# Kernel optimization log

Hardware: AMD Instinct MI355X
Metric: run time of the kernel (lower is better)

The kernel has to match this reference:

```python
import jax, jax.numpy as jnp
import numpy as np

H = 256       # hidden_dim
DICT = 30     # dict_size
SOS = 1       # symb2int['<sos>']

def gru_cell(x, h, Wih, Whh, bih, bhh):
    # PyTorch GRU cell math
    gi = x @ Wih.T + bih
    gh = h @ Whh.T + bhh
    ir, iz, inn = jnp.split(gi, 3, axis=-1)
    hr, hz, hn = jnp.split(gh, 3, axis=-1)
    r = jax.nn.sigmoid(ir + hr)
    z = jax.nn.sigmoid(iz + hz)
    n = jnp.tanh(inn + r * hn)
    return (1.0 - z) * n + z * h

def run_gru(xs, h0, Wih, Whh, bih, bhh):
    # xs: [T, B, F] -> outputs [T, B, Hc], final hidden [B, Hc]
    def step(h, x):
        h = gru_cell(x, h, Wih, Whh, bih, bhh)
        return h, h
    hT, out = jax.lax.scan(step, h0, xs)
    return out, hT

def setup_inputs() -> dict:
    key = jax.random.key(0)
    ks = jax.random.split(key, 24)
    B, T, L = 128, 512, 64
    se = 1.0 / np.sqrt(H)        # encoder GRU init scale
    sd = 1.0 / np.sqrt(2 * H)    # decoder GRU / linears scale
    def r(k, shape, sc):
        return jax.random.normal(k, shape, jnp.float32) * sc
    return {
        "x": jax.random.normal(ks[0], (B, T, 2), jnp.float32),
        "target_seq": jax.random.randint(ks[1], (B, L), 0, DICT),
        # encoder GRU, forward direction
        "enc_Wih_f": r(ks[2], (3 * H, 2), se), "enc_Whh_f": r(ks[3], (3 * H, H), se),
        "enc_bih_f": r(ks[4], (3 * H,), se),   "enc_bhh_f": r(ks[5], (3 * H,), se),
        # encoder GRU, backward direction
        "enc_Wih_b": r(ks[6], (3 * H, 2), se), "enc_Whh_b": r(ks[7], (3 * H, H), se),
        "enc_bih_b": r(ks[8], (3 * H,), se),   "enc_bhh_b": r(ks[9], (3 * H,), se),
        # decoder embedding + GRU (hidden 2H)
        "emb": r(ks[10], (DICT, H), 1.0),
        "dec_Wih": r(ks[11], (6 * H, H), sd),     "dec_Whh": r(ks[12], (6 * H, 2 * H), sd),
        "dec_bih": r(ks[13], (6 * H,), sd),       "dec_bhh": r(ks[14], (6 * H,), sd),
        # hidden2query, att_combine, fc
        "Wq": r(ks[15], (2 * H, 2 * H), sd), "bq": r(ks[16], (2 * H,), sd),
        "Wc": r(ks[17], (H, 4 * H), sd),     "bc": r(ks[18], (H,), sd),
        "Wf": r(ks[19], (DICT, H), se),      "bf": r(ks[20], (DICT,), se),
    }

def reference(x, target_seq,
              enc_Wih_f, enc_Whh_f, enc_bih_f, enc_bhh_f,
              enc_Wih_b, enc_Whh_b, enc_bih_b, enc_bhh_b,
              emb, dec_Wih, dec_Whh, dec_bih, dec_bhh,
              Wq, bq, Wc, bc, Wf, bf):
    B = x.shape[0]
    xs = jnp.transpose(x, (1, 0, 2))                # [T, B, 2]
    h0 = jnp.zeros((B, H), x.dtype)
    out_f, hf = run_gru(xs, h0, enc_Wih_f, enc_Whh_f, enc_bih_f, enc_bhh_f)
    out_b, hb = run_gru(xs[::-1], h0, enc_Wih_b, enc_Whh_b, enc_bih_b, enc_bhh_b)
    enc_out = jnp.concatenate([out_f, out_b[::-1]], axis=-1)  # [T, B, 2H]
    enc_out = jnp.transpose(enc_out, (1, 0, 2))               # [B, T, 2H]
    hidden = jnp.concatenate([hf, hb], axis=-1)               # [B, 2H]

    # teacher-forced decoder inputs: <sos>, target[0], ..., target[L-2]
    sos = jnp.full((B, 1), SOS, target_seq.dtype)
    toks = jnp.concatenate([sos, target_seq[:, :-1]], axis=1).T  # [L, B]

    def dec_step(h, tok):
        e = emb[tok]                                           # [B, H]
        h = gru_cell(e, h, dec_Wih, dec_Whh, dec_bih, dec_bhh) # [B, 2H]
        q = h @ Wq.T + bq                                      # hidden2query
        w = jax.nn.softmax(jnp.einsum('bh,bth->bt', q, enc_out), axis=-1)
        ctx = jnp.einsum('bt,bth->bh', w, enc_out)             # [B, 2H]
        o = jnp.concatenate([h, ctx], axis=-1) @ Wc.T + bc     # att_combine
        logits = o @ Wf.T + bf                                 # fc
        return h, (logits, w)

    hT, (logits, ws) = jax.lax.scan(dec_step, hidden, toks)
    vec_out = jnp.transpose(logits, (1, 0, 2))   # [B, L, DICT]
    attn = jnp.transpose(ws, (1, 2, 0))          # [B, T, L]
    return vec_out, hT[None], attn
```

## Files before the change

### kernel.cpp

```cpp
#include <hip/hip_runtime.h>
#include <hip/hip_bf16.h>

typedef unsigned int u32;
typedef unsigned short u16;
typedef _Float16 f16;
typedef f16 f16x2 __attribute__((ext_vector_type(2)));

#define BB 128
#define TT 512
#define HE 256
#define G3E 768
#define HD 512
#define G3D 1536
#define LL 64
#define NDICT 30
#define EMBD 256

__device__ __forceinline__ float fexp2(float v){
#if __has_builtin(__builtin_amdgcn_exp2f)
  return __builtin_amdgcn_exp2f(v);
#else
  return exp2f(v);
#endif
}
__device__ __forceinline__ float frcp(float v){
#if __has_builtin(__builtin_amdgcn_rcpf)
  return __builtin_amdgcn_rcpf(v);
#else
  return 1.f/v;
#endif
}
__device__ __forceinline__ float sigm(float v){
  return frcp(1.f + fexp2(-1.4426950408889634f*v));
}
__device__ __forceinline__ float ftanh(float v){
  float e = fexp2(fminf(v, 40.f)*2.8853901631790583f);
  return (e - 1.f)*frcp(e + 1.f);
}
__device__ __forceinline__ u16 f2h(float f){ return __builtin_bit_cast(u16, (f16)f); }
__device__ __forceinline__ float h2f(u16 b){ return (float)__builtin_bit_cast(f16, b); }
__device__ __forceinline__ u32 pkh2(float a, float b){
  u16 lo = __builtin_bit_cast(u16, (f16)a);
  u16 hi = __builtin_bit_cast(u16, (f16)b);
  return (u32)lo | ((u32)hi << 16);
}
__device__ __forceinline__ u32 pkrtz(float a, float b){
  return __builtin_bit_cast(u32, __builtin_amdgcn_cvt_pkrtz(a, b));
}
__device__ __forceinline__ f16x2 bc2(u32 v){ return __builtin_bit_cast(f16x2, v); }

__device__ __forceinline__ void unp8h(uint4 v, float* d){
  f16x2 p;
  p = bc2(v.x); d[0]=(float)p.x; d[1]=(float)p.y;
  p = bc2(v.y); d[2]=(float)p.x; d[3]=(float)p.y;
  p = bc2(v.z); d[4]=(float)p.x; d[5]=(float)p.y;
  p = bc2(v.w); d[6]=(float)p.x; d[7]=(float)p.y;
}
__device__ __forceinline__ ushort4 hpk4(float a, float b, float c, float d){
  ushort4 r; r.x=f2h(a); r.y=f2h(b); r.z=f2h(c); r.w=f2h(d); return r;
}

__device__ __forceinline__ float dot2a(u32 a, u32 b, float c){
  float d;
  asm("v_dot2_f32_f16 %0, %1, %2, %3" : "=v"(d) : "v"(a), "v"(b), "v"(c));
  return d;
}
__device__ __forceinline__ float dot2h(u32 a, u32 b, float acc){
  return dot2a(a, b, acc);
}
__device__ __forceinline__ void dot_u4(uint4 wv, uint4 hv, float& acc){
  acc = dot2a(wv.x, hv.x, acc);
  acc = dot2a(wv.y, hv.y, acc);
  acc = dot2a(wv.z, hv.z, acc);
  acc = dot2a(wv.w, hv.w, acc);
}

#define INNER8P(Q0,Q1)                                                  \
  _Pragma("unroll")                                                     \
  for (int kp = 0; kp < 16; ++kp){                                      \
    uint4 a2 = *(const uint4*)&A2_s[kp*68 + (Q0)*4];                    \
    uint4 b2 = *(const uint4*)&B2_s[kp*68 + (Q1)*4];                    \
    acc[0] =dot2h(a2.x,b2.x,acc[0]);  acc[1] =dot2h(a2.x,b2.y,acc[1]);  \
    acc[2] =dot2h(a2.x,b2.z,acc[2]);  acc[3] =dot2h(a2.x,b2.w,acc[3]);  \
    acc[4] =dot2h(a2.y,b2.x,acc[4]);  acc[5] =dot2h(a2.y,b2.y,acc[5]);  \
    acc[6] =dot2h(a2.y,b2.z,acc[6]);  acc[7] =dot2h(a2.y,b2.w,acc[7]);  \
    acc[8] =dot2h(a2.z,b2.x,acc[8]);  acc[9] =dot2h(a2.z,b2.y,acc[9]);  \
    acc[10]=dot2h(a2.z,b2.z,acc[10]); acc[11]=dot2h(a2.z,b2.w,acc[11]); \
    acc[12]=dot2h(a2.w,b2.x,acc[12]); acc[13]=dot2h(a2.w,b2.y,acc[13]); \
    acc[14]=dot2h(a2.w,b2.z,acc[14]); acc[15]=dot2h(a2.w,b2.w,acc[15]); \
  }

__global__ __launch_bounds__(256) void k_prep_pairT(const float* __restrict__ src,
                                                    u32* __restrict__ dst, int N, int K){
  int idx = blockIdx.x*256 + threadIdx.x;
  int KP = K >> 1;
  if (idx < N*KP){
    int n = idx / KP, kp = idx - n*KP;
    dst[(size_t)kp*N + n] = pkh2(src[(size_t)n*K + 2*kp], src[(size_t)n*K + 2*kp + 1]);
  }
}

__global__ __launch_bounds__(256) void k_prep_wenc(const float* __restrict__ WF,
                                                   const float* __restrict__ WB,
                                                   uint4* __restrict__ dst){
  int idx = blockIdx.x*256 + threadIdx.x;
  int dir = idx / 24576, rem = idx - dir*24576;
  int i = rem / 768, t = rem - i*768;
  int rg = t >> 3, cg = t & 7;
  int r = i >> 2, q = i & 3;
  const float* s = (dir ? WB : WF) + (size_t)(rg*8 + r)*HE + cg*32 + q*8;
  uint4 v; v.x=pkh2(s[0],s[1]); v.y=pkh2(s[2],s[3]); v.z=pkh2(s[4],s[5]); v.w=pkh2(s[6],s[7]);
  dst[idx] = v;
}

__global__ __launch_bounds__(256) void k_prep_wdec(const float* __restrict__ src,
                                                   uint4* __restrict__ dst){
  int idx = blockIdx.x*256 + threadIdx.x;
  int lane = idx & 63;
  int ci = lane & 7, kq = lane >> 3;
  int rest = idx >> 6;
  int u = rest & 7, g = (rest >> 3) % 3, cg = rest / 24;
  int row = g*512 + cg*8 + ci;
  int col = kq*64 + u*8;
  const float* s = src + (size_t)row*HD + col;
  uint4 v; v.x=pkh2(s[0],s[1]); v.y=pkh2(s[2],s[3]); v.z=pkh2(s[4],s[5]); v.w=pkh2(s[6],s[7]);
  dst[idx] = v;
}

__global__ __launch_bounds__(256) void k_gi_tab(const float* __restrict__ emb,
                                                const float* __restrict__ Wih,
                                                const float* __restrict__ bih,
                                                float* __restrict__ gi){
  int v = blockIdx.x, gy = blockIdx.y;
  int g = gy*256 + threadIdx.x;
  __shared__ float e_s[EMBD];
  if (threadIdx.x < EMBD) e_s[threadIdx.x] = emb[(size_t)v*EMBD + threadIdx.x];
  __syncthreads();
  const float4* w4 = (const float4*)(Wih + (size_t)g*EMBD);
  float acc = 0.f;
  #pragma unroll 8
  for (int k = 0; k < EMBD/4; ++k){
    float4 w = w4[k];
    float4 h = *(const float4*)&e_s[k*4];
    acc = fmaf(w.x,h.x,fmaf(w.y,h.y,fmaf(w.z,h.z,fmaf(w.w,h.w,acc))));
  }
  gi[(size_t)v*G3D + g] = acc + bih[g];
}

__global__ __launch_bounds__(256) void k_h0cvt(const float* __restrict__ src,
                                               f16* __restrict__ dst){
  int i = blockIdx.x*256 + threadIdx.x;
  dst[i] = (f16)src[i];
}

__global__ __launch_bounds__(768, 3) void k_enc_p(
    const float* __restrict__ x,
    const uint4* __restrict__ Wp,
    const float* __restrict__ WihF, const float* __restrict__ WihB,
    const float* __restrict__ bihF, const float* __restrict__ bhhF,
    const float* __restrict__ bihB, const float* __restrict__ bhhB,
    u16* __restrict__ enc_out, float* __restrict__ h0out)
{
  const int b   = blockIdx.x >> 1;
  const int dir = blockIdx.x & 1;
  const int j   = threadIdx.x;
  const int cg  = j & 7;
  const float* Wih = dir ? WihB : WihF;
  const float* bih = dir ? bihB : bihF;
  const float* bhh = dir ? bhhB : bhhF;

  __shared__ __align__(16) f16 h_pad[8*40];
  __shared__ float gh[2*HE];
  __shared__ float gin_s[HE], ghn_s[HE];

  uint4 w[32];
  {
    const uint4* wsrc = Wp + (size_t)dir*24576 + j;
    #pragma unroll
    for (int i = 0; i < 32; ++i) w[i] = wsrc[(size_t)i*768];
  }
  const float wv0r = Wih[j*2+0], wv1r = Wih[j*2+1];
  const float bi = bih[j], bh = bhh[j];
  const float badd = bi + bh;
  if (j < HE) h_pad[(j >> 5)*40 + (j & 31)] = (f16)0.f;
  float h_own = 0.f;
  const bool s0 = (cg & 1), s1 = (cg & 2), s2 = (cg & 4);
  __syncthreads();

  for (int t = 0; t < TT; ++t){
    const int tt = dir ? (TT-1-t) : t;
    const float x0 = x[((size_t)b*TT + tt)*2 + 0];
    const float x1 = x[((size_t)b*TT + tt)*2 + 1];

    const uint4* hv = (const uint4*)(h_pad + cg*40);
    uint4 h0 = hv[0], h1 = hv[1], h2 = hv[2], h3 = hv[3];
    float p[8];
    #pragma unroll
    for (int r = 0; r < 8; ++r){
      float a = 0.f;
      dot_u4(w[r*4+0], h0, a);
      dot_u4(w[r*4+1], h1, a);
      dot_u4(w[r*4+2], h2, a);
      dot_u4(w[r*4+3], h3, a);
      p[r] = a;
    }
    float q0 = (s0 ? p[1] : p[0]) + __shfl_xor(s0 ? p[0] : p[1], 1);
    float q1 = (s0 ? p[3] : p[2]) + __shfl_xor(s0 ? p[2] : p[3], 1);
    float q2 = (s0 ? p[5] : p[4]) + __shfl_xor(s0 ? p[4] : p[5], 1);
    float q3 = (s0 ? p[7] : p[6]) + __shfl_xor(s0 ? p[6] : p[7], 1);
    float r0 = (s1 ? q1 : q0) + __shfl_xor(s1 ? q0 : q1, 2);
    float r1 = (s1 ? q3 : q2) + __shfl_xor(s1 ? q2 : q3, 2);
    float tot = (s2 ? r1 : r0) + __shfl_xor(s2 ? r0 : r1, 4);

    const float xp = fmaf(wv0r, x0, wv1r*x1);
    if (j < 2*HE){
      gh[j] = tot + xp + badd;
    } else {
      ghn_s[j-2*HE] = tot + bh;
      gin_s[j-2*HE] = xp + bi;
    }
    __syncthreads();
    if (j < HE){
      float r = sigm(gh[j]);
      float z = sigm(gh[j+HE]);
      float n = ftanh(gin_s[j] + r*ghn_s[j]);
      float hnew = (1.f - z)*n + z*h_own;
      h_own = hnew;
      h_pad[(j >> 5)*40 + (j & 31)] = (f16)hnew;
      enc_out[((size_t)b*TT + tt)*HD + dir*HE + j] = f2h(hnew);
    }
    __syncthreads();
  }
  if (j < HE) h0out[(size_t)b*HD + dir*HE + j] = h_own;
}

__global__ __launch_bounds__(256, 2) void k_dstep(
    const int* __restrict__ tgt, const float* __restrict__ gi_tab,
    const uint4* __restrict__ Wd2, const float* __restrict__ bhh,
    const f16* __restrict__ h_prev, f16* __restrict__ h_next,
    float* __restrict__ Hall, int l)
{
  const int bg = blockIdx.x & 7, cg = blockIdx.x >> 3;
  const int tid = threadIdx.x;
  const int ci = tid & 7, kq = (tid >> 3) & 7, bq = tid >> 6;

  __shared__ __align__(16) f16 h_s[16][8][72];
  __shared__ float p_s[3][16][8][9];
  __shared__ int tok_s[16];

  uint4 w[24];
  {
    const uint4* wp = Wd2 + (size_t)cg*24*64 + (kq*8 + ci);
    #pragma unroll
    for (int i = 0; i < 24; ++i) w[i] = wp[(size_t)i*64];
  }
  {
    const uint4* hsrc = (const uint4*)(h_prev + (size_t)bg*16*HD);
    #pragma unroll
    for (int i = 0; i < 4; ++i){
      int idx = tid + i*256;
      int b = idx >> 6, w4 = idx & 63;
      int kq2 = w4 >> 3, off = w4 & 7;
      *(uint4*)&h_s[b][kq2][off*8] = hsrc[idx];
    }
  }
  if (tid < 16) tok_s[tid] = (l == 0) ? 1 : tgt[(size_t)(bg*16 + tid)*LL + l - 1];
  __syncthreads();

  #pragma unroll
  for (int nb = 0; nb < 4; ++nb){
    const int b = bq*4 + nb;
    const uint4* hv = (const uint4*)&h_s[b][kq][0];
    float x0 = 0.f, x1 = 0.f, x2 = 0.f;
    #pragma unroll
    for (int u = 0; u < 8; ++u){
      uint4 hh = hv[u];
      dot_u4(w[u],      hh, x0);
      dot_u4(w[8 + u],  hh, x1);
      dot_u4(w[16 + u], hh, x2);
    }
    p_s[0][b][ci][kq] = x0;
    p_s[1][b][ci][kq] = x1;
    p_s[2][b][ci][kq] = x2;
  }
  __syncthreads();

  if (tid < 128){
    const int b = tid >> 3, cl = tid & 7;
    const int C = cg*8 + cl;
    float s0 = 0.f, s1 = 0.f, s2 = 0.f;
    #pragma unroll
    for (int k = 0; k < 8; ++k){
      s0 += p_s[0][b][cl][k];
      s1 += p_s[1][b][cl][k];
      s2 += p_s[2][b][cl][k];
    }
    const int tok = tok_s[b];
    const float* gp = gi_tab + (size_t)tok*G3D + C;
    float r = sigm(gp[0]    + s0 + bhh[C]);
    float z = sigm(gp[HD]   + s1 + bhh[HD + C]);
    float n = ftanh(gp[2*HD] + r*(s2 + bhh[2*HD + C]));
    float hp = (float)h_s[b][C >> 6][C & 63];
    float hnew = (1.f - z)*n + z*hp;
    const int gb = bg*16 + b;
    h_next[(size_t)gb*HD + C] = (f16)hnew;
    Hall[((size_t)l*BB + gb)*HD + C] = hnew;
  }
}

__global__ __launch_bounds__(256) void k_query(const float* __restrict__ Hall,
                                               const u32* __restrict__ Wq2,
                                               const float* __restrict__ bq,
                                               u16* __restrict__ Qh){
  const int rt = blockIdx.x, nt = blockIdx.y;
  const int tid = threadIdx.x;
  __shared__ u32 A2_s[16*68];
  __shared__ u32 B2_s[16*68];
  const int rq = tid >> 4, nq = tid & 15;
  const int i = tid >> 2, jj = tid & 3;
  const int i3 = tid >> 4, n4 = tid & 15;
  float acc[16] = {};
  for (int kc = 0; kc < 16; ++kc){
    __syncthreads();
    {
      const float* src = Hall + (size_t)(rt*64 + i)*HD + kc*32 + jj*8;
      float4 v0 = *(const float4*)src, v1 = *(const float4*)(src+4);
      A2_s[(jj*4+0)*68+i] = pkrtz(v0.x, v0.y);
      A2_s[(jj*4+1)*68+i] = pkrtz(v0.z, v0.w);
      A2_s[(jj*4+2)*68+i] = pkrtz(v1.x, v1.y);
      A2_s[(jj*4+3)*68+i] = pkrtz(v1.z, v1.w);
    }
    {
      uint4 v = *(const uint4*)(Wq2 + (size_t)(kc*16 + i3)*HD + nt*64 + n4*4);
      *(uint4*)&B2_s[i3*68 + n4*4] = v;
    }
    __syncthreads();
    INNER8P(rq, nq)
  }
  const int n0 = nt*64 + nq*4;
  float4 bv = *(const float4*)&bq[n0];
  #pragma unroll
  for (int r = 0; r < 4; ++r){
    u16* dst = Qh + (size_t)(rt*64 + rq*4 + r)*HD + n0;
    *(ushort4*)dst = hpk4(acc[r*4+0]+bv.x, acc[r*4+1]+bv.y,
                          acc[r*4+2]+bv.z, acc[r*4+3]+bv.w);
  }
}

__global__ __launch_bounds__(256) void k_scores(const u16* __restrict__ Qh,
                                                const u16* __restrict__ enc,
                                                float* __restrict__ Sbuf){
  const int bI = blockIdx.x, tt = blockIdx.y;
  const int tid = threadIdx.x;
  __shared__ u32 A2_s[16*68];
  __shared__ u32 B2_s[16*68];
  const int lq = tid >> 4, tq = tid & 15;
  const int i = tid >> 2, jj = tid & 3;
  float acc[16] = {};
  for (int kc = 0; kc < 16; ++kc){
    __syncthreads();
    {
      uint4 va = *(const uint4*)(Qh + ((size_t)i*BB + bI)*HD + kc*32 + jj*8);
      A2_s[(jj*4+0)*68+i] = va.x;
      A2_s[(jj*4+1)*68+i] = va.y;
      A2_s[(jj*4+2)*68+i] = va.z;
      A2_s[(jj*4+3)*68+i] = va.w;
    }
    {
      uint4 vb = *(const uint4*)(enc + ((size_t)bI*TT + tt*64 + i)*HD + kc*32 + jj*8);
      B2_s[(jj*4+0)*68+i] = vb.x;
      B2_s[(jj*4+1)*68+i] = vb.y;
      B2_s[(jj*4+2)*68+i] = vb.z;
      B2_s[(jj*4+3)*68+i] = vb.w;
    }
    __syncthreads();
    INNER8P(lq, tq)
  }
  #pragma unroll
  for (int r = 0; r < 4; ++r){
    float4 o = make_float4(acc[r*4+0],acc[r*4+1],acc[r*4+2],acc[r*4+3]);
    *(float4*)&Sbuf[((size_t)bI*LL + lq*4+r)*TT + tt*64 + tq*4] = o;
  }
}

__global__ __launch_bounds__(64) void k_softmax(const float* __restrict__ Sbuf,
                                                u16* __restrict__ Ph){
  const int row = blockIdx.x;
  const int lane = threadIdx.x;
  const float* s = Sbuf + (size_t)row*TT;
  float v[8]; float m = -1e30f;
  #pragma unroll
  for (int i = 0; i < 8; ++i){ v[i] = s[lane + i*64]; m = fmaxf(m, v[i]); }
  #pragma unroll
  for (int o = 32; o; o >>= 1) m = fmaxf(m, __shfl_xor(m, o));
  float Z = 0.f;
  #pragma unroll
  for (int i = 0; i < 8; ++i){ v[i] = fexp2(1.4426950408889634f*(v[i] - m)); Z += v[i]; }
  #pragma unroll
  for (int o = 32; o; o >>= 1) Z += __shfl_xor(Z, o);
  float inv = frcp(Z);
  u16* p = Ph + (size_t)row*TT;
  #pragma unroll
  for (int i = 0; i < 8; ++i) p[lane + i*64] = f2h(v[i]*inv);
}

__global__ __launch_bounds__(256) void k_attn_tr(const u16* __restrict__ Ph,
                                                 float* __restrict__ att){
  const int bI = blockIdx.x, tt = blockIdx.y;
  const int tid = threadIdx.x;
  __shared__ u16 tile[64][72];
  {
    const int i = tid >> 2, jj = tid & 3;
    #pragma unroll
    for (int rep = 0; rep < 2; ++rep){
      int ch = jj + rep*4;
      uint4 v = *(const uint4*)(Ph + ((size_t)bI*LL + i)*TT + tt*64 + ch*8);
      *(uint4*)&tile[i][ch*8] = v;
    }
  }
  __syncthreads();
  const int t = tid >> 2, jl = tid & 3;
  #pragma unroll
  for (int rep = 0; rep < 4; ++rep){
    int l0 = jl*16 + rep*4;
    float4 o;
    o.x = h2f(tile[l0+0][t]); o.y = h2f(tile[l0+1][t]);
    o.z = h2f(tile[l0+2][t]); o.w = h2f(tile[l0+3][t]);
    *(float4*)&att[((size_t)bI*TT + tt*64 + t)*LL + l0] = o;
  }
}

__global__ __launch_bounds__(256) void k_ctx(const u16* __restrict__ Ph,
                                             const u16* __restrict__ enc,
                                             u16* __restrict__ ctxh){
  const int bI = blockIdx.x, nt = blockIdx.y;
  const int tid = threadIdx.x;
  __shared__ u32 A2_s[16*68];
  __shared__ u32 B2_s[16*68];
  const int lq = tid >> 4, nq = tid & 15;
  const int i = tid >> 2, jj = tid & 3;
  const int q = tid >> 4, n4 = tid & 15;
  float acc[16] = {};
  for (int tc = 0; tc < 16; ++tc){
    __syncthreads();
    {
      uint4 va = *(const uint4*)(Ph + ((size_t)bI*LL + i)*TT + tc*32 + jj*8);
      A2_s[(jj*4+0)*68+i] = va.x;
      A2_s[(jj*4+1)*68+i] = va.y;
      A2_s[(jj*4+2)*68+i] = va.z;
      A2_s[(jj*4+3)*68+i] = va.w;
    }
    {
      const int t0 = tc*32 + 2*q;
      const int n0 = nt*64 + n4*4;
      uint2 a = *(const uint2*)(enc + ((size_t)bI*TT + t0)*HD + n0);
      uint2 b = *(const uint2*)(enc + ((size_t)bI*TT + t0 + 1)*HD + n0);
      B2_s[q*68 + n4*4 + 0] = (a.x & 0xffffu) | (b.x << 16);
      B2_s[q*68 + n4*4 + 1] = (a.x >> 16) | (b.x & 0xffff0000u);
      B2_s[q*68 + n4*4 + 2] = (a.y & 0xffffu) | (b.y << 16);
      B2_s[q*68 + n4*4 + 3] = (a.y >> 16) | (b.y & 0xffff0000u);
    }
    __syncthreads();
    INNER8P(lq, nq)
  }
  const int n0 = nt*64 + nq*4;
  #pragma unroll
  for (int r = 0; r < 4; ++r){
    int ll = lq*4 + r;
    u16* dst = ctxh + ((size_t)ll*BB + bI)*HD + n0;
    *(ushort4*)dst = hpk4(acc[r*4+0], acc[r*4+1], acc[r*4+2], acc[r*4+3]);
  }
}

__global__ __launch_bounds__(256) void k_outc(const float* __restrict__ Hall,
                                              const u16* __restrict__ ctxh,
                                              const u32* __restrict__ Wc2,
                                              const float* __restrict__ bc,
                                              float* __restrict__ obuf){
  const int rt = blockIdx.x, nt = blockIdx.y;
  const int tid = threadIdx.x;
  __shared__ u32 A2_s[16*68];
  __shared__ u32 B2_s[16*68];
  const int rq = tid >> 4, nq = tid & 15;
  const int i = tid >> 2, jj = tid & 3;
  const int i3 = tid >> 4, n4 = tid & 15;
  float acc[16] = {};
  for (int kc = 0; kc < 32; ++kc){
    __syncthreads();
    if (kc < 16){
      const float* src = Hall + (size_t)(rt*64 + i)*HD + kc*32 + jj*8;
      float4 v0 = *(const float4*)src, v1 = *(const float4*)(src+4);
      A2_s[(jj*4+0)*68+i] = pkrtz(v0.x, v0.y);
      A2_s[(jj*4+1)*68+i] = pkrtz(v0.z, v0.w);
      A2_s[(jj*4+2)*68+i] = pkrtz(v1.x, v1.y);
      A2_s[(jj*4+3)*68+i] = pkrtz(v1.z, v1.w);
    } else {
      uint4 v = *(const uint4*)(ctxh + (size_t)(rt*64 + i)*HD + (kc-16)*32 + jj*8);
      A2_s[(jj*4+0)*68+i] = v.x;
      A2_s[(jj*4+1)*68+i] = v.y;
      A2_s[(jj*4+2)*68+i] = v.z;
      A2_s[(jj*4+3)*68+i] = v.w;
    }
    {
      uint4 v = *(const uint4*)(Wc2 + (size_t)(kc*16 + i3)*256 + nt*64 + n4*4);
      *(uint4*)&B2_s[i3*68 + n4*4] = v;
    }
    __syncthreads();
    INNER8P(rq, nq)
  }
  const int n0 = nt*64 + nq*4;
  float4 bv = *(const float4*)&bc[n0];
  #pragma unroll
  for (int r = 0; r < 4; ++r){
    float4 o = make_float4(acc[r*4+0]+bv.x, acc[r*4+1]+bv.y,
                           acc[r*4+2]+bv.z, acc[r*4+3]+bv.w);
    *(float4*)&obuf[(size_t)(rt*64 + rq*4 + r)*256 + n0] = o;
  }
}

__global__ __launch_bounds__(256) void k_fc(const float* __restrict__ obuf,
                                            const float* __restrict__ Wf,
                                            const float* __restrict__ bfv,
                                            float* __restrict__ out_vec){
  const int rt = blockIdx.x;
  const int tid = threadIdx.x;
  __shared__ float w_s[30*260];
  for (int rr = 0; rr < 30; ++rr) w_s[rr*260 + tid] = Wf[(size_t)rr*256 + tid];
  __syncthreads();
  const int rl = tid >> 2, dq = tid & 3;
  const int r = rt*64 + rl;
  float acc[8] = {};
  for (int k = 0; k < 256; k += 4){
    float4 o4 = *(const float4*)&obuf[(size_t)r*256 + k];
    #pragma unroll
    for (int jq = 0; jq < 8; ++jq){
      int d = dq*8 + jq;
      if (d < 30){
        float4 w4 = *(const float4*)&w_s[d*260 + k];
        acc[jq] = fmaf(o4.x,w4.x,fmaf(o4.y,w4.y,fmaf(o4.z,w4.z,fmaf(o4.w,w4.w,acc[jq]))));
      }
    }
  }
  const int b = r & 127, l = r >> 7;
  #pragma unroll
  for (int jq = 0; jq < 8; ++jq){
    int d = dq*8 + jq;
    if (d < 30) out_vec[((size_t)b*LL + l)*NDICT + d] = acc[jq] + bfv[d];
  }
}

__global__ __launch_bounds__(256) void k_copy(const float* __restrict__ src,
                                              float* __restrict__ dst, int n){
  int i = blockIdx.x*256 + threadIdx.x;
  if (i < n) dst[i] = src[i];
}

extern "C" void kernel_launch(void* const* d_in, const int* in_sizes, int n_in,
                              void* d_out, int out_size, void* d_ws, size_t ws_size,
                              hipStream_t stream)
{
  const float* x     = (const float*)d_in[0];
  const int*   tgt   = (const int*)  d_in[1];
  const float* eWihF = (const float*)d_in[2];
  const float* eWhhF = (const float*)d_in[3];
  const float* ebihF = (const float*)d_in[4];
  const float* ebhhF = (const float*)d_in[5];
  const float* eWihB = (const float*)d_in[6];
  const float* eWhhB = (const float*)d_in[7];
  const float* ebihB = (const float*)d_in[8];
  const float* ebhhB = (const float*)d_in[9];
  const float* emb   = (const float*)d_in[10];
  const float* dWih  = (const float*)d_in[11];
  const float* dWhh  = (const float*)d_in[12];
  const float* dbih  = (const float*)d_in[13];
  const float* dbhh  = (const float*)d_in[14];
  const float* Wq    = (const float*)d_in[15];
  const float* bq    = (const float*)d_in[16];
  const float* Wc    = (const float*)d_in[17];
  const float* bc    = (const float*)d_in[18];
  const float* Wf    = (const float*)d_in[19];
  const float* bfv   = (const float*)d_in[20];

  char* w = (char*)d_ws;
  uint4* Wpenc = (uint4*)w; w += 786432;
  uint4* Wpdec = (uint4*)w; w += 1572864;
  u32*   Wq2   = (u32*)w;  w += 524288;
  u32*   Wc2   = (u32*)w;  w += 524288;
  float* gi_t  = (float*)w; w += 184320;
  float* h0buf = (float*)w; w += 262144;
  f16*   h16A  = (f16*)w; w += 131072;
  f16*   h16B  = (f16*)w; w += 131072;
  float* Hall  = (float*)w; w += 16777216;
  u16*   Qh    = (u16*)w;
  u16*   Ph    = (u16*)w; w += 8388608;
  float* Sbuf  = (float*)w;
  u16*   ctxh  = (u16*)w; w += 8388608;
  float* obuf  = (float*)w; w += 8388608;
  u16*   ench  = (u16*)w; w += 67108864;

  float* out     = (float*)d_out;
  float* out_vec = out;
  float* out_hT  = out + (size_t)BB*LL*NDICT;
  float* out_att = out_hT + (size_t)BB*HD;

  k_prep_wenc<<<192, 256, 0, stream>>>(eWhhF, eWhhB, Wpenc);
  k_prep_wdec<<<384, 256, 0, stream>>>(dWhh, Wpdec);
  k_prep_pairT<<<512, 256, 0, stream>>>(Wq, Wq2, HD, HD);
  k_prep_pairT<<<512, 256, 0, stream>>>(Wc, Wc2, 256, 1024);
  k_gi_tab<<<dim3(NDICT, 6), 256, 0, stream>>>(emb, dWih, dbih, gi_t);

  k_enc_p<<<BB*2, G3E, 0, stream>>>(x, Wpenc, eWihF, eWihB,
                                    ebihF, ebhhF, ebihB, ebhhB, ench, h0buf);

  k_h0cvt<<<256, 256, 0, stream>>>(h0buf, h16A);
  for (int l = 0; l < LL; ++l){
    const f16* hp = (l & 1) ? h16B : h16A;
    f16*       hn = (l & 1) ? h16A : h16B;
    k_dstep<<<512, 256, 0, stream>>>(tgt, gi_t, Wpdec, dbhh, hp, hn, Hall, l);
  }

  k_query<<<dim3(128,8), 256, 0, stream>>>(Hall, Wq2, bq, Qh);
  k_scores<<<dim3(128,8), 256, 0, stream>>>(Qh, ench, Sbuf);
  k_softmax<<<BB*LL, 64, 0, stream>>>(Sbuf, Ph);
  k_attn_tr<<<dim3(128,8), 256, 0, stream>>>(Ph, out_att);
  k_ctx<<<dim3(128,8), 256, 0, stream>>>(Ph, ench, ctxh);
  k_outc<<<dim3(128,4), 256, 0, stream>>>(Hall, ctxh, Wc2, bc, obuf);
  k_fc<<<BB, 256, 0, stream>>>(obuf, Wf, bfv, out_vec);
  k_copy<<<(BB*HD+255)/256, 256, 0, stream>>>(Hall + (size_t)63*BB*HD, out_hT, BB*HD);
}
```

Measured before the change: 1.244 ms.

## Restructure encoder GRU step to 512 threads with LDS partial-sum reduction

The encoder recurrence kernel moves from 768 to 512 threads per block. Each thread now holds 48 weight vectors and computes 12 gate rows over a 32-column slice. The old shuffle-based reduction is replaced by writing partial dot products to shared memory, after which 256 threads sum them and apply the gate math. This trades more register pressure and extra LDS traffic for fewer waves and no cross-lane shuffles. The weight prep layout and the dot2 helper (now a builtin when available) are updated to match.

```diff
diff --git a/kernel.cpp b/kernel.cpp
--- a/kernel.cpp
+++ b/kernel.cpp
@@ -49,30 +49,24 @@
 }
 __device__ __forceinline__ f16x2 bc2(u32 v){ return __builtin_bit_cast(f16x2, v); }
 
-__device__ __forceinline__ void unp8h(uint4 v, float* d){
-  f16x2 p;
-  p = bc2(v.x); d[0]=(float)p.x; d[1]=(float)p.y;
-  p = bc2(v.y); d[2]=(float)p.x; d[3]=(float)p.y;
-  p = bc2(v.z); d[4]=(float)p.x; d[5]=(float)p.y;
-  p = bc2(v.w); d[6]=(float)p.x; d[7]=(float)p.y;
-}
 __device__ __forceinline__ ushort4 hpk4(float a, float b, float c, float d){
   ushort4 r; r.x=f2h(a); r.y=f2h(b); r.z=f2h(c); r.w=f2h(d); return r;
 }
 
-__device__ __forceinline__ float dot2a(u32 a, u32 b, float c){
+__device__ __forceinline__ float dot2h(u32 a, u32 b, float acc){
+#if __has_builtin(__builtin_amdgcn_fdot2)
+  return __builtin_amdgcn_fdot2(bc2(a), bc2(b), acc, false);
+#else
   float d;
-  asm("v_dot2_f32_f16 %0, %1, %2, %3" : "=v"(d) : "v"(a), "v"(b), "v"(c));
+  asm("v_dot2_f32_f16 %0, %1, %2, %3" : "=v"(d) : "v"(a), "v"(b), "v"(acc));
   return d;
-}
-__device__ __forceinline__ float dot2h(u32 a, u32 b, float acc){
-  return dot2a(a, b, acc);
+#endif
 }
 __device__ __forceinline__ void dot_u4(uint4 wv, uint4 hv, float& acc){
-  acc = dot2a(wv.x, hv.x, acc);
-  acc = dot2a(wv.y, hv.y, acc);
-  acc = dot2a(wv.z, hv.z, acc);
-  acc = dot2a(wv.w, hv.w, acc);
+  acc = dot2h(wv.x, hv.x, acc);
+  acc = dot2h(wv.y, hv.y, acc);
+  acc = dot2h(wv.z, hv.z, acc);
+  acc = dot2h(wv.w, hv.w, acc);
 }
 
 #define INNER8P(Q0,Q1)                                                  \
@@ -105,10 +99,10 @@
                                                    uint4* __restrict__ dst){
   int idx = blockIdx.x*256 + threadIdx.x;
   int dir = idx / 24576, rem = idx - dir*24576;
-  int i = rem / 768, t = rem - i*768;
+  int i = rem >> 9, t = rem & 511;
   int rg = t >> 3, cg = t & 7;
-  int r = i >> 2, q = i & 3;
-  const float* s = (dir ? WB : WF) + (size_t)(rg*8 + r)*HE + cg*32 + q*8;
+  int k = i >> 2, q = i & 3;
+  const float* s = (dir ? WB : WF) + (size_t)(rg*12 + k)*HE + cg*32 + q*8;
   uint4 v; v.x=pkh2(s[0],s[1]); v.y=pkh2(s[2],s[3]); v.z=pkh2(s[4],s[5]); v.w=pkh2(s[6],s[7]);
   dst[idx] = v;
 }
@@ -153,7 +147,7 @@
   dst[i] = (f16)src[i];
 }
 
-__global__ __launch_bounds__(768, 3) void k_enc_p(
+__global__ __launch_bounds__(512, 2) void k_enc_p(
     const float* __restrict__ x,
     const uint4* __restrict__ Wp,
     const float* __restrict__ WihF, const float* __restrict__ WihB,
@@ -163,28 +157,36 @@
 {
   const int b   = blockIdx.x >> 1;
   const int dir = blockIdx.x & 1;
-  const int j   = threadIdx.x;
-  const int cg  = j & 7;
+  const int tid = threadIdx.x;
+  const int cg  = tid & 7;
   const float* Wih = dir ? WihB : WihF;
   const float* bih = dir ? bihB : bihF;
   const float* bhh = dir ? bhhB : bhhF;
 
   __shared__ __align__(16) f16 h_pad[8*40];
-  __shared__ float gh[2*HE];
-  __shared__ float gin_s[HE], ghn_s[HE];
-
-  uint4 w[32];
+  __shared__ float p_lds[G3E*9];
+
+  uint4 w4[48];
   {
-    const uint4* wsrc = Wp + (size_t)dir*24576 + j;
+    const uint4* wsrc = Wp + (size_t)dir*24576 + tid;
     #pragma unroll
-    for (int i = 0; i < 32; ++i) w[i] = wsrc[(size_t)i*768];
-  }
-  const float wv0r = Wih[j*2+0], wv1r = Wih[j*2+1];
-  const float bi = bih[j], bh = bhh[j];
-  const float badd = bi + bh;
-  if (j < HE) h_pad[(j >> 5)*40 + (j & 31)] = (f16)0.f;
+    for (int i = 0; i < 48; ++i) w4[i] = wsrc[(size_t)i*512];
+  }
+  float wv0r=0.f,wv1r=0.f,wv0z=0.f,wv1z=0.f,wv0n=0.f,wv1n=0.f;
+  float br=0.f,bz=0.f,bin=0.f,bhn=0.f;
   float h_own = 0.f;
-  const bool s0 = (cg & 1), s1 = (cg & 2), s2 = (cg & 4);
+  if (tid < HE){
+    const int j = tid;
+    wv0r = Wih[j*2];         wv1r = Wih[j*2+1];
+    wv0z = Wih[(j+HE)*2];    wv1z = Wih[(j+HE)*2+1];
+    wv0n = Wih[(j+2*HE)*2];  wv1n = Wih[(j+2*HE)*2+1];
+    br  = bih[j] + bhh[j];
+    bz  = bih[j+HE] + bhh[j+HE];
+    bin = bih[j+2*HE];
+    bhn = bhh[j+2*HE];
+    h_pad[(j >> 5)*40 + (j & 31)] = (f16)0.f;
+  }
+  const int rowbase = (tid >> 3)*12;
   __syncthreads();
 
   for (int t = 0; t < TT; ++t){
@@ -192,38 +194,34 @@
     const float x0 = x[((size_t)b*TT + tt)*2 + 0];
     const float x1 = x[((size_t)b*TT + tt)*2 + 1];
 
-    const uint4* hv = (const uint4*)(h_pad + cg*40);
-    uint4 h0 = hv[0], h1 = hv[1], h2 = hv[2], h3 = hv[3];
-    float p[8];
-    #pragma unroll
-    for (int r = 0; r < 8; ++r){
-      float a = 0.f;
-      dot_u4(w[r*4+0], h0, a);
-      dot_u4(w[r*4+1], h1, a);
-      dot_u4(w[r*4+2], h2, a);
-      dot_u4(w[r*4+3], h3, a);
-      p[r] = a;
-    }
-    float q0 = (s0 ? p[1] : p[0]) + __shfl_xor(s0 ? p[0] : p[1], 1);
-    float q1 = (s0 ? p[3] : p[2]) + __shfl_xor(s0 ? p[2] : p[3], 1);
-    float q2 = (s0 ? p[5] : p[4]) + __shfl_xor(s0 ? p[4] : p[5], 1);
-    float q3 = (s0 ? p[7] : p[6]) + __shfl_xor(s0 ? p[6] : p[7], 1);
-    float r0 = (s1 ? q1 : q0) + __shfl_xor(s1 ? q0 : q1, 2);
-    float r1 = (s1 ? q3 : q2) + __shfl_xor(s1 ? q2 : q3, 2);
-    float tot = (s2 ? r1 : r0) + __shfl_xor(s2 ? r0 : r1, 4);
-
-    const float xp = fmaf(wv0r, x0, wv1r*x1);
-    if (j < 2*HE){
-      gh[j] = tot + xp + badd;
-    } else {
-      ghn_s[j-2*HE] = tot + bh;
-      gin_s[j-2*HE] = xp + bi;
-    }
-    __syncthreads();
-    if (j < HE){
-      float r = sigm(gh[j]);
-      float z = sigm(gh[j+HE]);
-      float n = ftanh(gin_s[j] + r*ghn_s[j]);
+    {
+      const uint4* hv = (const uint4*)(h_pad + cg*40);
+      uint4 h0 = hv[0], h1 = hv[1], h2 = hv[2], h3 = hv[3];
+      #pragma unroll
+      for (int k = 0; k < 12; ++k){
+        float a = 0.f;
+        dot_u4(w4[k*4+0], h0, a);
+        dot_u4(w4[k*4+1], h1, a);
+        dot_u4(w4[k*4+2], h2, a);
+        dot_u4(w4[k*4+3], h3, a);
+        p_lds[(rowbase + k)*9 + cg] = a;
+      }
+    }
+    __syncthreads();
+    if (tid < HE){
+      const int j = tid;
+      float sr=0.f, sz=0.f, sn=0.f;
+      #pragma unroll
+      for (int k = 0; k < 8; ++k){
+        sr += p_lds[j*9 + k];
+        sz += p_lds[(j+HE)*9 + k];
+        sn += p_lds[(j+2*HE)*9 + k];
+      }
+      float gr = sr + fmaf(wv0r, x0, wv1r*x1) + br;
+      float gz = sz + fmaf(wv0z, x0, wv1z*x1) + bz;
+      float gni = fmaf(wv0n, x0, wv1n*x1) + bin;
+      float r = sigm(gr), z = sigm(gz);
+      float n = ftanh(gni + r*(sn + bhn));
       float hnew = (1.f - z)*n + z*h_own;
       h_own = hnew;
       h_pad[(j >> 5)*40 + (j & 31)] = (f16)hnew;
@@ -231,7 +229,7 @@
     }
     __syncthreads();
   }
-  if (j < HE) h0out[(size_t)b*HD + dir*HE + j] = h_own;
+  if (tid < HE) h0out[(size_t)b*HD + dir*HE + tid] = h_own;
 }
 
 __global__ __launch_bounds__(256, 2) void k_dstep(
@@ -609,7 +607,7 @@
   k_prep_pairT<<<512, 256, 0, stream>>>(Wc, Wc2, 256, 1024);
   k_gi_tab<<<dim3(NDICT, 6), 256, 0, stream>>>(emb, dWih, dbih, gi_t);
 
-  k_enc_p<<<BB*2, G3E, 0, stream>>>(x, Wpenc, eWihF, eWihB,
+  k_enc_p<<<BB*2, 512, 0, stream>>>(x, Wpenc, eWihF, eWihB,
                                     ebihF, ebhhF, ebihB, ebhhB, ench, h0buf);
 
   k_h0cvt<<<256, 256, 0, stream>>>(h0buf, h16A);
```

After: 1.164 ms (median of 2 runs). 6.4% less time.
